# Kernel optimization log

Hardware: AMD Instinct MI355X
Metric: run time of the kernel (lower is better)

## Reference

```python
import jax, jax.numpy as jnp
import numpy as np

NUM_GROUPS = 8   # also the per-group channel count (C = NUM_GROUPS**2)
NUM_LEVELS = 4
RADIUS = 4


def setup_inputs() -> dict:
    key = jax.random.key(0)
    k1, k2, k3 = jax.random.split(key, 3)
    B, C, H, W = 2, 64, 80, 160
    fmap1 = jax.random.normal(k1, (B, C, H, W), dtype=jnp.float32)
    fmap2 = jax.random.normal(k2, (B, C, H, W), dtype=jnp.float32)
    coords = jax.random.uniform(k3, (B, 1, H, W), dtype=jnp.float32) * (W - 1)
    return {"fmap1": fmap1, "fmap2": fmap2, "coords": coords}


def _build_cost_volume(fmap1, fmap2):
    # group-wise correlation: torch.split(fmap, G, dim=1) -> chunks of G channels
    B, C, H, W = fmap1.shape
    G = NUM_GROUPS
    gc = NUM_GROUPS  # chunk size; C == G * gc
    f1 = fmap1.reshape(B, G, gc, H, W)
    f2 = fmap2.reshape(B, G, gc, H, W)
    # cv[b,g,h,w,v] = sum_c f1[b,g,c,h,w] * f2[b,g,c,h,v] / sqrt(gc)
    cv = jnp.einsum('bgchw,bgchv->bghwv', f1, f2) / jnp.sqrt(jnp.float32(gc))
    return cv  # (B, G, H, W, W2)


def _pyramid(cv, n_levels):
    pyr = [cv]
    for _ in range(n_levels):
        B, G, H, W, Wl = cv.shape
        cv = cv.reshape(B, G, H, W, Wl // 2, 2).mean(-1)  # avg_pool1d(k=2,s=2)
        pyr.append(cv)
    return pyr


def _linear_sample(cv, x):
    # cv: (B,G,H,W,Wl) 1D signals; x: (B,G,H,W,K) sample positions
    Wl = cv.shape[-1]
    x0 = jnp.floor(x)
    w1 = x - x0
    i0 = x0.astype(jnp.int32)
    i1 = i0 + 1
    g0 = jnp.take_along_axis(cv, jnp.clip(i0, 0, Wl - 1), axis=-1)
    g1 = jnp.take_along_axis(cv, jnp.clip(i1, 0, Wl - 1), axis=-1)
    v0 = (i0 >= 0) & (i0 < Wl)
    v1 = (i1 >= 0) & (i1 < Wl)
    zero = jnp.zeros((), cv.dtype)
    return jnp.where(v0, g0 * (1.0 - w1), zero) + jnp.where(v1, g1 * w1, zero)


def reference(fmap1, fmap2, coords):
    B, _, H, W = coords.shape
    G, r = NUM_GROUPS, RADIUS
    K = 2 * r + 1
    cv = _build_cost_volume(fmap1, fmap2)
    geo = cv  # regularizer_3d treated as identity (see notes)
    feat_pyr = _pyramid(cv, NUM_LEVELS)
    geo_pyr = _pyramid(geo, NUM_LEVELS)
    dx = jnp.linspace(-r, r, K, dtype=jnp.float32)  # (K,)
    c = coords[:, 0][:, None]  # (B,1,H,W), broadcasts over groups
    outs = []
    for i in range(NUM_LEVELS):
        coords_lvl = c[..., None] / (2.0 ** i) + dx  # (B,1,H,W,K)
        coords_lvl = jnp.broadcast_to(coords_lvl, (B, G, H, W, K))
        for pyr in (feat_pyr, geo_pyr):
            s = _linear_sample(pyr[i], coords_lvl)            # (B,G,H,W,K)
            outs.append(s.transpose(0, 2, 3, 1, 4).reshape(B, H, W, G * K))
    out = jnp.concatenate(outs, axis=-1)  # (B,H,W, 2*L*G*K)
    return out.transpose(0, 3, 1, 2).astype(jnp.float32)
```

## Files before the change

kernel.cpp:

```cpp
#include <hip/hip_runtime.h>


namespace {
constexpr int B_ = 2, C_ = 64, H_ = 80, W_ = 160;
constexpr int G_ = 8, GC_ = 8, L_ = 4, K_ = 9, R_ = 4;
constexpr int HW_ = H_ * W_;
constexpr int NCH_ = 2 * L_ * G_ * K_;
constexpr int TPB = 320;
constexpr int NBINS = 160 + 80 + 40 + 20;
constexpr float INV_SQRT_GC = 0.35355339059327373f;
}

__global__ __launch_bounds__(TPB, 5) void gacv_kernel(
    const float* __restrict__ fmap1, const float* __restrict__ fmap2,
    const float* __restrict__ coords, float* __restrict__ out) {
  __shared__ __align__(16) float pA[NBINS * 4];
  __shared__ __align__(16) float pB[NBINS * 4];

  const int tid = threadIdx.x;
  const int bid = blockIdx.x;
  const int half = bid & 1;
  const int rid = bid >> 1;
  const int h = rid % H_;
  const int bg = rid / H_;
  const int g = bg % G_;
  const int b = bg / G_;

  const float* f2base = fmap2 + (size_t)(b * C_ + g * GC_) * HW_ + h * W_;
  for (int idx = tid; idx < W_ * GC_; idx += TPB) {
    int c = idx & 7;
    int v = idx >> 3;
    float val = f2base[c * HW_ + v];
    if (c < 4) pA[v * 4 + c] = val;
    else       pB[v * 4 + (c - 4)] = val;
  }
  __syncthreads();
  for (int idx = tid; idx < 80 * 4; idx += TPB) {
    int t = idx >> 2, c = idx & 3;
    pA[(160 + t) * 4 + c] = 0.5f * (pA[(2 * t) * 4 + c] + pA[(2 * t + 1) * 4 + c]);
    pB[(160 + t) * 4 + c] = 0.5f * (pB[(2 * t) * 4 + c] + pB[(2 * t + 1) * 4 + c]);
  }
  __syncthreads();
  for (int idx = tid; idx < 40 * 4; idx += TPB) {
    int t = idx >> 2, c = idx & 3;
    pA[(240 + t) * 4 + c] = 0.5f * (pA[(160 + 2 * t) * 4 + c] + pA[(160 + 2 * t + 1) * 4 + c]);
    pB[(240 + t) * 4 + c] = 0.5f * (pB[(160 + 2 * t) * 4 + c] + pB[(160 + 2 * t + 1) * 4 + c]);
  }
  __syncthreads();
  for (int idx = tid; idx < 20 * 4; idx += TPB) {
    int t = idx >> 2, c = idx & 3;
    pA[(280 + t) * 4 + c] = 0.5f * (pA[(240 + 2 * t) * 4 + c] + pA[(240 + 2 * t + 1) * 4 + c]);
    pB[(280 + t) * 4 + c] = 0.5f * (pB[(240 + 2 * t) * 4 + c] + pB[(240 + 2 * t + 1) * 4 + c]);
  }
  __syncthreads();

  const int w_local = tid % 80;
  const int lvl = tid / 80;
  const int w = half * 80 + w_local;

  float f1v[GC_];
  const float* f1base = fmap1 + (size_t)(b * C_ + g * GC_) * HW_ + h * W_ + w;
#pragma unroll
  for (int c = 0; c < GC_; ++c) f1v[c] = f1base[c * HW_] * INV_SQRT_GC;

  const float cx = coords[(b * H_ + h) * W_ + w];
  const float xl = ldexpf(cx, -lvl);
  const int Wl = W_ >> lvl;
  const int ofs = (lvl == 0) ? 0 : (lvl == 1) ? 160 : (lvl == 2) ? 240 : 280;
  const float F = floorf(xl);
  const int fi = (int)F;
  const float w1 = xl - F;
  const float w0 = 1.0f - w1;

  float T[2 * R_ + 2];
#pragma unroll
  for (int j = 0; j < 2 * R_ + 2; ++j) {
    int t = fi - R_ + j;
    int tc = min(max(t, 0), Wl - 1);
    const float4 a = *(const float4*)(pA + (ofs + tc) * 4);
    const float4 q = *(const float4*)(pB + (ofs + tc) * 4);
    float s = f1v[0] * a.x + f1v[1] * a.y + f1v[2] * a.z + f1v[3] * a.w +
              f1v[4] * q.x + f1v[5] * q.y + f1v[6] * q.z + f1v[7] * q.w;
    T[j] = (t == tc) ? s : 0.0f;
  }

  float* outb = out + (size_t)b * NCH_ * HW_ + h * W_ + w;
  const int chBase = lvl * (2 * G_ * K_) + g * K_;
#pragma unroll
  for (int k = 0; k < K_; ++k) {
    float val = w0 * T[k] + w1 * T[k + 1];
    outb[(size_t)(chBase + k) * HW_] = val;
    outb[(size_t)(chBase + G_ * K_ + k) * HW_] = val;
  }
}

extern "C" void kernel_launch(void* const* d_in, const int* in_sizes, int n_in,
                              void* d_out, int out_size, void* d_ws, size_t ws_size,
                              hipStream_t stream) {
  const float* fmap1 = (const float*)d_in[0];
  const float* fmap2 = (const float*)d_in[1];
  const float* coords = (const float*)d_in[2];
  float* out = (float*)d_out;
  gacv_kernel<<<dim3(B_ * G_ * H_ * 2), dim3(TPB), 0, stream>>>(fmap1, fmap2, coords, out);
}
```

Baseline: 86.78 us.

## Store fmap2 pyramid in LDS as fp16 half2 channel-pair planes

Converts the shared-memory pyramid of fmap2 from two fp32 float4-interleaved arrays to four planes of half2 (channel pairs), so the LDS footprint is halved. Pooling levels are computed with packed half arithmetic, one element per thread. The gather then reads four 32-bit half2 values per bin instead of two 128-bit float4 loads. The launch-bounds occupancy hint is removed. This cuts LDS traffic and footprint, but it loses precision in the correlation values and adds conversion instructions.

```diff
diff --git a/kernel.cpp b/kernel.cpp
--- a/kernel.cpp
+++ b/kernel.cpp
@@ -1,4 +1,5 @@
 #include <hip/hip_runtime.h>
+#include <hip/hip_fp16.h>
 
 
 namespace {
@@ -11,11 +12,10 @@
 constexpr float INV_SQRT_GC = 0.35355339059327373f;
 }
 
-__global__ __launch_bounds__(TPB, 5) void gacv_kernel(
+__global__ __launch_bounds__(TPB) void gacv_kernel(
     const float* __restrict__ fmap1, const float* __restrict__ fmap2,
     const float* __restrict__ coords, float* __restrict__ out) {
-  __shared__ __align__(16) float pA[NBINS * 4];
-  __shared__ __align__(16) float pB[NBINS * 4];
+  __shared__ __half2 pln[4][NBINS];
 
   const int tid = threadIdx.x;
   const int bid = blockIdx.x;
@@ -27,30 +27,28 @@
   const int b = bg / G_;
 
   const float* f2base = fmap2 + (size_t)(b * C_ + g * GC_) * HW_ + h * W_;
-  for (int idx = tid; idx < W_ * GC_; idx += TPB) {
-    int c = idx & 7;
-    int v = idx >> 3;
-    float val = f2base[c * HW_ + v];
-    if (c < 4) pA[v * 4 + c] = val;
-    else       pB[v * 4 + (c - 4)] = val;
+  for (int idx = tid; idx < 4 * W_; idx += TPB) {
+    int v = idx % W_;
+    int pair = idx / W_;
+    float lo = f2base[(2 * pair) * HW_ + v];
+    float hi = f2base[(2 * pair + 1) * HW_ + v];
+    pln[pair][v] = __floats2half2_rn(lo, hi);
   }
   __syncthreads();
-  for (int idx = tid; idx < 80 * 4; idx += TPB) {
-    int t = idx >> 2, c = idx & 3;
-    pA[(160 + t) * 4 + c] = 0.5f * (pA[(2 * t) * 4 + c] + pA[(2 * t + 1) * 4 + c]);
-    pB[(160 + t) * 4 + c] = 0.5f * (pB[(2 * t) * 4 + c] + pB[(2 * t + 1) * 4 + c]);
+  const __half2 halfc = __float2half2_rn(0.5f);
+  {
+    int t = tid % 80, pair = tid / 80;
+    pln[pair][160 + t] = __hmul2(__hadd2(pln[pair][2 * t], pln[pair][2 * t + 1]), halfc);
   }
   __syncthreads();
-  for (int idx = tid; idx < 40 * 4; idx += TPB) {
-    int t = idx >> 2, c = idx & 3;
-    pA[(240 + t) * 4 + c] = 0.5f * (pA[(160 + 2 * t) * 4 + c] + pA[(160 + 2 * t + 1) * 4 + c]);
-    pB[(240 + t) * 4 + c] = 0.5f * (pB[(160 + 2 * t) * 4 + c] + pB[(160 + 2 * t + 1) * 4 + c]);
+  if (tid < 160) {
+    int t = tid % 40, pair = tid / 40;
+    pln[pair][240 + t] = __hmul2(__hadd2(pln[pair][160 + 2 * t], pln[pair][160 + 2 * t + 1]), halfc);
   }
   __syncthreads();
-  for (int idx = tid; idx < 20 * 4; idx += TPB) {
-    int t = idx >> 2, c = idx & 3;
-    pA[(280 + t) * 4 + c] = 0.5f * (pA[(240 + 2 * t) * 4 + c] + pA[(240 + 2 * t + 1) * 4 + c]);
-    pB[(280 + t) * 4 + c] = 0.5f * (pB[(240 + 2 * t) * 4 + c] + pB[(240 + 2 * t + 1) * 4 + c]);
+  if (tid < 80) {
+    int t = tid % 20, pair = tid / 20;
+    pln[pair][280 + t] = __hmul2(__hadd2(pln[pair][240 + 2 * t], pln[pair][240 + 2 * t + 1]), halfc);
   }
   __syncthreads();
 
@@ -66,7 +64,7 @@
   const float cx = coords[(b * H_ + h) * W_ + w];
   const float xl = ldexpf(cx, -lvl);
   const int Wl = W_ >> lvl;
-  const int ofs = (lvl == 0) ? 0 : (lvl == 1) ? 160 : (lvl == 2) ? 240 : 280;
+  const int ofs = 320 - (320 >> lvl);
   const float F = floorf(xl);
   const int fi = (int)F;
   const float w1 = xl - F;
@@ -77,10 +75,13 @@
   for (int j = 0; j < 2 * R_ + 2; ++j) {
     int t = fi - R_ + j;
     int tc = min(max(t, 0), Wl - 1);
-    const float4 a = *(const float4*)(pA + (ofs + tc) * 4);
-    const float4 q = *(const float4*)(pB + (ofs + tc) * 4);
-    float s = f1v[0] * a.x + f1v[1] * a.y + f1v[2] * a.z + f1v[3] * a.w +
-              f1v[4] * q.x + f1v[5] * q.y + f1v[6] * q.z + f1v[7] * q.w;
+    int bi = ofs + tc;
+    float2 c0 = __half22float2(pln[0][bi]);
+    float2 c1 = __half22float2(pln[1][bi]);
+    float2 c2 = __half22float2(pln[2][bi]);
+    float2 c3 = __half22float2(pln[3][bi]);
+    float s = f1v[0] * c0.x + f1v[1] * c0.y + f1v[2] * c1.x + f1v[3] * c1.y +
+              f1v[4] * c2.x + f1v[5] * c2.y + f1v[6] * c3.x + f1v[7] * c3.y;
     T[j] = (t == tc) ? s : 0.0f;
   }
 
```

After: 85.44 us, median of 2. Within noise of the previous version (-1.5%).
